# Kernel optimization log

Hardware: AMD Instinct MI355X
Metric: run time of the kernel (lower is better)

Reference implementation:

```python
import jax, jax.numpy as jnp
import numpy as np

NUM_EXPERTS = 64
D_MODEL = 1024
N_TOKENS = 4096
TOP_K = 2
CAPACITY = 512


def setup_inputs() -> dict:
    key = jax.random.key(0)
    k1, k2, k3 = jax.random.split(key, 3)
    x = jax.random.normal(k1, (N_TOKENS, D_MODEL), dtype=jnp.float32)
    gate_w = 0.02 * jax.random.normal(k2, (NUM_EXPERTS, D_MODEL), dtype=jnp.float32)
    expert_w = 0.02 * jax.random.normal(k3, (NUM_EXPERTS, D_MODEL, D_MODEL), dtype=jnp.float32)
    return {"x": x, "gate_w": gate_w, "expert_w": expert_w}


def reference(x, gate_w, expert_w):
    N, d = x.shape
    E = gate_w.shape[0]
    # --- gating: top-2 + softmax over the two selected logits ---
    logits = x @ gate_w.T                         # [N, E]
    top_logits, top_idx = jax.lax.top_k(logits, TOP_K)
    weights = jax.nn.softmax(top_logits, axis=-1) # [N, 2]
    flat_idx = top_idx.reshape(-1)                # [2N], expert per token-slot
    flat_w = weights.reshape(-1)                  # [2N]
    tokens = jnp.repeat(x, TOP_K, axis=0)         # [2N, d] (repeat_interleave)
    # --- dispatch: stable sort by expert, position within expert ---
    order = jnp.argsort(flat_idx)                 # stable
    se = flat_idx[order]                          # sorted expert ids
    starts = jnp.searchsorted(se, jnp.arange(E))  # first row of each expert
    pos = jnp.arange(se.shape[0]) - starts[se]    # slot within expert
    buf = jnp.zeros((E, CAPACITY, d), x.dtype).at[se, pos].set(tokens[order], mode="drop")
    # --- per-expert GEMM (Linear no bias: y = x @ W.T) ---
    eout = jnp.einsum("ecd,efd->ecf", buf, expert_w)  # [E, C, d]
    # --- combine: gather back, scale by gate weight, unsort, sum top-2 ---
    out_sorted = eout[se, jnp.clip(pos, 0, CAPACITY - 1)] * flat_w[order][:, None]
    combined = jnp.zeros_like(tokens).at[order].set(out_sorted)
    return combined.reshape(N, TOP_K, d).sum(axis=1)
```

## Files before the change

### kernel.cpp

```cpp
#include <hip/hip_runtime.h>
#include <stdint.h>

#define N_TOKENS 4096
#define D_MODEL  1024
#define NUM_EXP  64
#define CAP      512

typedef unsigned short u16;
typedef __bf16 bf16x8 __attribute__((ext_vector_type(8)));
typedef float  f32x4  __attribute__((ext_vector_type(4)));
typedef const __attribute__((address_space(1))) void* as1cvp;
typedef __attribute__((address_space(3))) void*       as3vp;

__device__ __forceinline__ uint32_t f2bf_bits(float f) {
  union { float f; uint32_t u; } c; c.f = f;
  uint32_t u = c.u;
  u += 0x7fffu + ((u >> 16) & 1u);
  return u >> 16;
}

__global__ __launch_bounds__(256) void gate_fused_kernel(
    const float* __restrict__ x, const float* __restrict__ gw,
    u16* __restrict__ xb, int* __restrict__ cnt,
    int* __restrict__ tok, float* __restrict__ wts)
{
  const int t0  = blockIdx.x * 16;
  const int tid = threadIdx.x;
  const int tt = tid >> 4, eg = tid & 15;

  __shared__ float4 xs[16][32];
  __shared__ float4 gws[64][32];
  __shared__ float  lg[16][64];

  float acc[4] = {0.f, 0.f, 0.f, 0.f};

  for (int kc = 0; kc < 8; ++kc) {
    const int k0 = kc * 128;
    __syncthreads();
    #pragma unroll
    for (int i = 0; i < 2; ++i) {
      int idx = tid + i * 256;
      int r = idx >> 5, c = idx & 31;
      float4 v = *(const float4*)&x[(size_t)(t0 + r) * D_MODEL + k0 + c * 4];
      xs[r][c ^ r] = v;
      uint32_t lo = f2bf_bits(v.x) | (f2bf_bits(v.y) << 16);
      uint32_t hi = f2bf_bits(v.z) | (f2bf_bits(v.w) << 16);
      *(uint2*)&xb[(size_t)(t0 + r) * D_MODEL + k0 + c * 4] = make_uint2(lo, hi);
    }
    #pragma unroll
    for (int i = 0; i < 8; ++i) {
      int idx = tid + i * 256;
      int r = idx >> 5, c = idx & 31;
      gws[r][c ^ (r & 31)] = *(const float4*)&gw[(size_t)r * D_MODEL + k0 + c * 4];
    }
    __syncthreads();
    #pragma unroll
    for (int c = 0; c < 32; ++c) {
      float4 xa = xs[tt][c ^ tt];
      #pragma unroll
      for (int j = 0; j < 4; ++j) {
        int e = eg * 4 + j;
        float4 wv = gws[e][c ^ (e & 31)];
        acc[j] += xa.x * wv.x; acc[j] += xa.y * wv.y;
        acc[j] += xa.z * wv.z; acc[j] += xa.w * wv.w;
      }
    }
  }
  #pragma unroll
  for (int j = 0; j < 4; ++j) lg[tt][eg * 4 + j] = acc[j];
  __syncthreads();

  if (tid < 16) {
    float b1 = -3.4e38f; int e1 = 0;
    #pragma unroll
    for (int e = 0; e < 64; ++e) { float v = lg[tid][e]; if (v > b1) { b1 = v; e1 = e; } }
    float b2 = -3.4e38f; int e2 = 0;
    #pragma unroll
    for (int e = 0; e < 64; ++e) { float v = lg[tid][e]; if (e != e1 && v > b2) { b2 = v; e2 = e; } }
    float ex = expf(b2 - b1);
    float w1 = 1.0f / (1.0f + ex);
    float w2 = ex   / (1.0f + ex);
    int t = t0 + tid;
    int p = atomicAdd(&cnt[e1], 1);
    if (p < CAP) { tok[e1 * CAP + p] = t; wts[e1 * CAP + p] = w1; }
    p = atomicAdd(&cnt[e2], 1);
    if (p < CAP) { tok[e2 * CAP + p] = t; wts[e2 * CAP + p] = w2; }
  }
}

__global__ __launch_bounds__(512) void expert_gemm_kernel(
    const u16* __restrict__ xb, const float* __restrict__ ew,
    const int* __restrict__ cnt, const int* __restrict__ tok,
    const float* __restrict__ wts, float* __restrict__ out)
{
  const int e = blockIdx.z;
  int ne = cnt[e]; ne = ne > CAP ? CAP : ne;
  const int m0 = blockIdx.y * 128;
  if (m0 >= ne) return;
  const int n0 = blockIdx.x * 128;
  const int tid = threadIdx.x;
  const int wid = tid >> 6, lane = tid & 63;
  const int wm = wid & 1, wn = wid >> 1;

  __shared__ u16  Alds[2][128 * 64];
  __shared__ u16  Blds[2][128 * 64];
  __shared__ int   tokL[128];
  __shared__ float wL[128];

  if (tid < 128) {
    int g = m0 + tid;
    bool v = g < ne;
    tokL[tid] = v ? tok[e * CAP + g] : 0;
    wL[tid]   = v ? wts[e * CAP + g] : 0.f;
  }
  __syncthreads();

  const u16* asrc[2];
  #pragma unroll
  for (int i = 0; i < 2; ++i) {
    int idx = tid + i * 512;
    int r = idx >> 3, c = idx & 7;
    asrc[i] = xb + (size_t)tokL[r] * D_MODEL + (c ^ (r & 7)) * 8;
  }
  const float* Wb = ew + (size_t)e * D_MODEL * D_MODEL + (size_t)n0 * D_MODEL;
  const float* bsrc[4]; int boff[4];
  #pragma unroll
  for (int i = 0; i < 4; ++i) {
    int idx = tid + i * 512;
    int r = idx >> 4, c = idx & 15;
    bsrc[i] = Wb + (size_t)r * D_MODEL + c * 4;
    boff[i] = r * 128 + (((c >> 1) ^ (r & 7)) << 4) + (c & 1) * 8;
  }

  #pragma unroll
  for (int i = 0; i < 2; ++i)
    __builtin_amdgcn_global_load_lds((as1cvp)(asrc[i]),
                                     (as3vp)((char*)&Alds[0][0] + (tid + i * 512) * 16), 16, 0, 0);
  {
    float4 bv[4];
    #pragma unroll
    for (int i = 0; i < 4; ++i) bv[i] = *(const float4*)(bsrc[i]);
    #pragma unroll
    for (int i = 0; i < 4; ++i) {
      uint32_t lo = f2bf_bits(bv[i].x) | (f2bf_bits(bv[i].y) << 16);
      uint32_t hi = f2bf_bits(bv[i].z) | (f2bf_bits(bv[i].w) << 16);
      *(uint2*)((char*)&Blds[0][0] + boff[i]) = make_uint2(lo, hi);
    }
  }
  __syncthreads();

  f32x4 acc[4][2] = {};

  for (int t = 0; t < 16; ++t) {
    const char* ldsA = (const char*)&Alds[t & 1][0];
    const char* ldsB = (const char*)&Blds[t & 1][0];
    char* ldsAn = (char*)&Alds[(t & 1) ^ 1][0];
    char* ldsBn = (char*)&Blds[(t & 1) ^ 1][0];

    float4 bv[4];
    if (t < 15) {
      const int kn = (t + 1) * 64;
      #pragma unroll
      for (int i = 0; i < 2; ++i)
        __builtin_amdgcn_global_load_lds((as1cvp)(asrc[i] + kn),
                                         (as3vp)(ldsAn + (tid + i * 512) * 16), 16, 0, 0);
      #pragma unroll
      for (int i = 0; i < 4; ++i) bv[i] = *(const float4*)(bsrc[i] + kn);
    }

    #pragma unroll
    for (int kk = 0; kk < 2; ++kk) {
      const int kbyte = kk * 64 + (lane >> 4) * 16;
      bf16x8 a[4], b[2];
      #pragma unroll
      for (int mi = 0; mi < 4; ++mi) {
        int r = wm * 64 + mi * 16 + (lane & 15);
        a[mi] = *(const bf16x8*)(ldsA + r * 128 + (kbyte ^ ((r & 7) << 4)));
      }
      #pragma unroll
      for (int nj = 0; nj < 2; ++nj) {
        int r = wn * 32 + nj * 16 + (lane & 15);
        b[nj] = *(const bf16x8*)(ldsB + r * 128 + (kbyte ^ ((r & 7) << 4)));
      }
      #pragma unroll
      for (int mi = 0; mi < 4; ++mi)
        #pragma unroll
        for (int nj = 0; nj < 2; ++nj)
          acc[mi][nj] = __builtin_amdgcn_mfma_f32_16x16x32_bf16(a[mi], b[nj], acc[mi][nj], 0, 0, 0);
    }

    if (t < 15) {
      #pragma unroll
      for (int i = 0; i < 4; ++i) {
        uint32_t lo = f2bf_bits(bv[i].x) | (f2bf_bits(bv[i].y) << 16);
        uint32_t hi = f2bf_bits(bv[i].z) | (f2bf_bits(bv[i].w) << 16);
        *(uint2*)(ldsBn + boff[i]) = make_uint2(lo, hi);
      }
    }
    __syncthreads();
  }

  #pragma unroll
  for (int mi = 0; mi < 4; ++mi) {
    #pragma unroll
    for (int r4 = 0; r4 < 4; ++r4) {
      int rl = wm * 64 + mi * 16 + (lane >> 4) * 4 + r4;
      if (m0 + rl < ne) {
        float wg = wL[rl];
        size_t dbase = (size_t)tokL[rl] * D_MODEL + n0 + wn * 32 + (lane & 15);
        #pragma unroll
        for (int nj = 0; nj < 2; ++nj)
          unsafeAtomicAdd(&out[dbase + nj * 16], acc[mi][nj][r4] * wg);
      }
    }
  }
}

extern "C" void kernel_launch(void* const* d_in, const int* in_sizes, int n_in,
                              void* d_out, int out_size, void* d_ws, size_t ws_size,
                              hipStream_t stream) {
  const float* x  = (const float*)d_in[0];
  const float* gw = (const float*)d_in[1];
  const float* ew = (const float*)d_in[2];
  float* out = (float*)d_out;
  char* ws = (char*)d_ws;
  int*   cnt = (int*)(ws + 0);
  int*   tok = (int*)(ws + 1024);
  float* wts = (float*)(ws + 132096);
  u16*   xb  = (u16*)  (ws + 263168);

  hipMemsetAsync(cnt, 0, 64 * sizeof(int), stream);
  hipMemsetAsync(out, 0, (size_t)N_TOKENS * D_MODEL * sizeof(float), stream);
  gate_fused_kernel<<<256, 256, 0, stream>>>(x, gw, xb, cnt, tok, wts);
  expert_gemm_kernel<<<dim3(8, 4, 64), 512, 0, stream>>>(xb, ew, cnt, tok, wts, out);
}
```

Before: 535.6 us.

## Retile expert GEMM to 256x64 tiles with fp32 weights loaded direct to LDS

Measured after the change: 499.0 us. 1.07x faster.

```diff
diff --git a/kernel.cpp b/kernel.cpp
--- a/kernel.cpp
+++ b/kernel.cpp
@@ -24,23 +24,21 @@
     u16* __restrict__ xb, int* __restrict__ cnt,
     int* __restrict__ tok, float* __restrict__ wts)
 {
-  const int t0  = blockIdx.x * 16;
+  const int t0  = blockIdx.x * 8;
   const int tid = threadIdx.x;
-  const int tt = tid >> 4, eg = tid & 15;
-
-  __shared__ float4 xs[16][32];
+  const int tt = tid >> 5, eg = tid & 31;
+
+  __shared__ float4 xs[8][32];
   __shared__ float4 gws[64][32];
-  __shared__ float  lg[16][64];
-
-  float acc[4] = {0.f, 0.f, 0.f, 0.f};
+  __shared__ float  lg[8][64];
+
+  float acc[2] = {0.f, 0.f};
 
   for (int kc = 0; kc < 8; ++kc) {
     const int k0 = kc * 128;
     __syncthreads();
-    #pragma unroll
-    for (int i = 0; i < 2; ++i) {
-      int idx = tid + i * 256;
-      int r = idx >> 5, c = idx & 31;
+    {
+      int r = tid >> 5, c = tid & 31;
       float4 v = *(const float4*)&x[(size_t)(t0 + r) * D_MODEL + k0 + c * 4];
       xs[r][c ^ r] = v;
       uint32_t lo = f2bf_bits(v.x) | (f2bf_bits(v.y) << 16);
@@ -58,19 +56,19 @@
     for (int c = 0; c < 32; ++c) {
       float4 xa = xs[tt][c ^ tt];
       #pragma unroll
-      for (int j = 0; j < 4; ++j) {
-        int e = eg * 4 + j;
-        float4 wv = gws[e][c ^ (e & 31)];
+      for (int j = 0; j < 2; ++j) {
+        int ee = eg * 2 + j;
+        float4 wv = gws[ee][c ^ (ee & 31)];
         acc[j] += xa.x * wv.x; acc[j] += xa.y * wv.y;
         acc[j] += xa.z * wv.z; acc[j] += xa.w * wv.w;
       }
     }
   }
   #pragma unroll
-  for (int j = 0; j < 4; ++j) lg[tt][eg * 4 + j] = acc[j];
+  for (int j = 0; j < 2; ++j) lg[tt][eg * 2 + j] = acc[j];
   __syncthreads();
 
-  if (tid < 16) {
+  if (tid < 8) {
     float b1 = -3.4e38f; int e1 = 0;
     #pragma unroll
     for (int e = 0; e < 64; ++e) { float v = lg[tid][e]; if (v > b1) { b1 = v; e1 = e; } }
@@ -88,26 +86,28 @@
   }
 }
 
-__global__ __launch_bounds__(512) void expert_gemm_kernel(
+__global__ __launch_bounds__(256, 3) void expert_gemm_kernel(
     const u16* __restrict__ xb, const float* __restrict__ ew,
     const int* __restrict__ cnt, const int* __restrict__ tok,
     const float* __restrict__ wts, float* __restrict__ out)
 {
   const int e = blockIdx.z;
   int ne = cnt[e]; ne = ne > CAP ? CAP : ne;
-  const int m0 = blockIdx.y * 128;
+  const int m0 = blockIdx.y * 256;
   if (m0 >= ne) return;
-  const int n0 = blockIdx.x * 128;
+  const int nloc = (ne - m0) > 256 ? 256 : (ne - m0);
+  const int ner  = (nloc + 63) & ~63;
+  const int n0 = blockIdx.x * 64;
   const int tid = threadIdx.x;
   const int wid = tid >> 6, lane = tid & 63;
-  const int wm = wid & 1, wn = wid >> 1;
-
-  __shared__ u16  Alds[2][128 * 64];
-  __shared__ u16  Blds[2][128 * 64];
-  __shared__ int   tokL[128];
-  __shared__ float wL[128];
-
-  if (tid < 128) {
+  const bool live = (wid * 64) < nloc;
+
+  __shared__ __align__(16) u16   Alds[256 * 64];
+  __shared__ __align__(16) float Blds[64 * 64];
+  __shared__ int   tokL[256];
+  __shared__ float wL[256];
+
+  {
     int g = m0 + tid;
     bool v = g < ne;
     tokL[tid] = v ? tok[e * CAP + g] : 0;
@@ -115,102 +115,84 @@
   }
   __syncthreads();
 
-  const u16* asrc[2];
+  int arow[8]; const u16* asrc[8];
   #pragma unroll
-  for (int i = 0; i < 2; ++i) {
-    int idx = tid + i * 512;
+  for (int i = 0; i < 8; ++i) {
+    int idx = tid + i * 256;
     int r = idx >> 3, c = idx & 7;
+    arow[i] = r;
     asrc[i] = xb + (size_t)tokL[r] * D_MODEL + (c ^ (r & 7)) * 8;
   }
-  const float* Wb = ew + (size_t)e * D_MODEL * D_MODEL + (size_t)n0 * D_MODEL;
-  const float* bsrc[4]; int boff[4];
+  const float* Wb = ew + (size_t)e * D_MODEL * D_MODEL;
+  const float* bsrc[4];
   #pragma unroll
   for (int i = 0; i < 4; ++i) {
-    int idx = tid + i * 512;
-    int r = idx >> 4, c = idx & 15;
-    bsrc[i] = Wb + (size_t)r * D_MODEL + c * 4;
-    boff[i] = r * 128 + (((c >> 1) ^ (r & 7)) << 4) + (c & 1) * 8;
-  }
-
-  #pragma unroll
-  for (int i = 0; i < 2; ++i)
-    __builtin_amdgcn_global_load_lds((as1cvp)(asrc[i]),
-                                     (as3vp)((char*)&Alds[0][0] + (tid + i * 512) * 16), 16, 0, 0);
-  {
-    float4 bv[4];
-    #pragma unroll
-    for (int i = 0; i < 4; ++i) bv[i] = *(const float4*)(bsrc[i]);
-    #pragma unroll
-    for (int i = 0; i < 4; ++i) {
-      uint32_t lo = f2bf_bits(bv[i].x) | (f2bf_bits(bv[i].y) << 16);
-      uint32_t hi = f2bf_bits(bv[i].z) | (f2bf_bits(bv[i].w) << 16);
-      *(uint2*)((char*)&Blds[0][0] + boff[i]) = make_uint2(lo, hi);
-    }
-  }
-  __syncthreads();
-
-  f32x4 acc[4][2] = {};
-
-  for (int t = 0; t < 16; ++t) {
-    const char* ldsA = (const char*)&Alds[t & 1][0];
-    const char* ldsB = (const char*)&Blds[t & 1][0];
-    char* ldsAn = (char*)&Alds[(t & 1) ^ 1][0];
-    char* ldsBn = (char*)&Blds[(t & 1) ^ 1][0];
-
-    float4 bv[4];
-    if (t < 15) {
-      const int kn = (t + 1) * 64;
+    int idx = tid + i * 256;
+    int r = idx >> 4, c16 = idx & 15;
+    int c32 = c16 >> 1;
+    int cs16 = ((c32 ^ (r & 7)) << 1) | (c16 & 1);
+    bsrc[i] = Wb + (size_t)(n0 + r) * D_MODEL + cs16 * 4;
+  }
+
+  f32x4 acc[4][4] = {};
+
+  for (int k0 = 0; k0 < D_MODEL; k0 += 64) {
+    __syncthreads();
+    #pragma unroll
+    for (int i = 0; i < 8; ++i)
+      if (arow[i] < ner)
+        __builtin_amdgcn_global_load_lds((as1cvp)(asrc[i] + k0),
+                                         (as3vp)(Alds + (tid + i * 256) * 8), 16, 0, 0);
+    #pragma unroll
+    for (int i = 0; i < 4; ++i)
+      __builtin_amdgcn_global_load_lds((as1cvp)(bsrc[i] + k0),
+                                       (as3vp)((char*)Blds + (tid + i * 256) * 16), 16, 0, 0);
+    __syncthreads();
+
+    if (live) {
       #pragma unroll
-      for (int i = 0; i < 2; ++i)
-        __builtin_amdgcn_global_load_lds((as1cvp)(asrc[i] + kn),
-                                         (as3vp)(ldsAn + (tid + i * 512) * 16), 16, 0, 0);
+      for (int kk = 0; kk < 2; ++kk) {
+        const int kbyte = kk * 64 + (lane >> 4) * 16;
+        bf16x8 a[4], b[4];
+        #pragma unroll
+        for (int mi = 0; mi < 4; ++mi) {
+          int r = wid * 64 + mi * 16 + (lane & 15);
+          a[mi] = *(const bf16x8*)((const char*)Alds + r * 128 + (kbyte ^ ((r & 7) << 4)));
+        }
+        #pragma unroll
+        for (int nj = 0; nj < 4; ++nj) {
+          int r = nj * 16 + (lane & 15);
+          int c32 = kk * 4 + (lane >> 4);
+          const float* p = (const float*)((const char*)Blds + r * 256 + ((c32 ^ (r & 7)) << 5));
+          f32x4 lo = *(const f32x4*)p;
+          f32x4 hi = *(const f32x4*)(p + 4);
+          b[nj][0] = (__bf16)lo[0]; b[nj][1] = (__bf16)lo[1];
+          b[nj][2] = (__bf16)lo[2]; b[nj][3] = (__bf16)lo[3];
+          b[nj][4] = (__bf16)hi[0]; b[nj][5] = (__bf16)hi[1];
+          b[nj][6] = (__bf16)hi[2]; b[nj][7] = (__bf16)hi[3];
+        }
+        #pragma unroll
+        for (int mi = 0; mi < 4; ++mi)
+          #pragma unroll
+          for (int nj = 0; nj < 4; ++nj)
+            acc[mi][nj] = __builtin_amdgcn_mfma_f32_16x16x32_bf16(a[mi], b[nj], acc[mi][nj], 0, 0, 0);
+      }
+    }
+  }
+
+  if (live) {
+    #pragma unroll
+    for (int mi = 0; mi < 4; ++mi) {
       #pragma unroll
-      for (int i = 0; i < 4; ++i) bv[i] = *(const float4*)(bsrc[i] + kn);
-    }
-
-    #pragma unroll
-    for (int kk = 0; kk < 2; ++kk) {
-      const int kbyte = kk * 64 + (lane >> 4) * 16;
-      bf16x8 a[4], b[2];
-      #pragma unroll
-      for (int mi = 0; mi < 4; ++mi) {
-        int r = wm * 64 + mi * 16 + (lane & 15);
-        a[mi] = *(const bf16x8*)(ldsA + r * 128 + (kbyte ^ ((r & 7) << 4)));
-      }
-      #pragma unroll
-      for (int nj = 0; nj < 2; ++nj) {
-        int r = wn * 32 + nj * 16 + (lane & 15);
-        b[nj] = *(const bf16x8*)(ldsB + r * 128 + (kbyte ^ ((r & 7) << 4)));
-      }
-      #pragma unroll
-      for (int mi = 0; mi < 4; ++mi)
-        #pragma unroll
-        for (int nj = 0; nj < 2; ++nj)
-          acc[mi][nj] = __builtin_amdgcn_mfma_f32_16x16x32_bf16(a[mi], b[nj], acc[mi][nj], 0, 0, 0);
-    }
-
-    if (t < 15) {
-      #pragma unroll
-      for (int i = 0; i < 4; ++i) {
-        uint32_t lo = f2bf_bits(bv[i].x) | (f2bf_bits(bv[i].y) << 16);
-        uint32_t hi = f2bf_bits(bv[i].z) | (f2bf_bits(bv[i].w) << 16);
-        *(uint2*)(ldsBn + boff[i]) = make_uint2(lo, hi);
-      }
-    }
-    __syncthreads();
-  }
-
-  #pragma unroll
-  for (int mi = 0; mi < 4; ++mi) {
-    #pragma unroll
-    for (int r4 = 0; r4 < 4; ++r4) {
-      int rl = wm * 64 + mi * 16 + (lane >> 4) * 4 + r4;
-      if (m0 + rl < ne) {
-        float wg = wL[rl];
-        size_t dbase = (size_t)tokL[rl] * D_MODEL + n0 + wn * 32 + (lane & 15);
-        #pragma unroll
-        for (int nj = 0; nj < 2; ++nj)
-          unsafeAtomicAdd(&out[dbase + nj * 16], acc[mi][nj][r4] * wg);
+      for (int r4 = 0; r4 < 4; ++r4) {
+        int rl = wid * 64 + mi * 16 + (lane >> 4) * 4 + r4;
+        if (rl < nloc) {
+          float wg = wL[rl];
+          size_t dbase = (size_t)tokL[rl] * D_MODEL + n0 + (lane & 15);
+          #pragma unroll
+          for (int nj = 0; nj < 4; ++nj)
+            unsafeAtomicAdd(&out[dbase + nj * 16], acc[mi][nj][r4] * wg);
+        }
       }
     }
   }
@@ -231,6 +213,6 @@
 
   hipMemsetAsync(cnt, 0, 64 * sizeof(int), stream);
   hipMemsetAsync(out, 0, (size_t)N_TOKENS * D_MODEL * sizeof(float), stream);
-  gate_fused_kernel<<<256, 256, 0, stream>>>(x, gw, xb, cnt, tok, wts);
-  expert_gemm_kernel<<<dim3(8, 4, 64), 512, 0, stream>>>(xb, ew, cnt, tok, wts, out);
-}
+  gate_fused_kernel<<<512, 256, 0, stream>>>(x, gw, xb, cnt, tok, wts);
+  expert_gemm_kernel<<<dim3(16, 2, 64), 256, 0, stream>>>(xb, ew, cnt, tok, wts, out);
+}
```
